# Kernel tuning notes

Hardware: AMD Instinct MI355X
Metric: run time of the kernel (lower is better)

## Reference

```python
import jax, jax.numpy as jnp
import numpy as np


def setup_inputs() -> dict:
    key = jax.random.key(0)
    k1, k2, k3 = jax.random.split(key, 3)
    B, L, C, D, V = 8, 512, 4000, 512, 10000
    x = jax.random.uniform(k1, (B, L, C), dtype=jnp.float32)            # dense char n-gram features
    W_proj = jax.random.normal(k2, (D, C), dtype=jnp.float32) * 0.02     # Linear(char_vsize, d_vec), no bias
    emb_matrix = jax.random.uniform(k3, (V, D), dtype=jnp.float32,
                                    minval=-0.1, maxval=0.1)             # QueryEmb latent embedding table
    return {"x": x, "W_proj": W_proj, "emb_matrix": emb_matrix}


def reference(x, W_proj, emb_matrix):
    # charEmbedder: tanh(Linear(x)) per sentence -> vectorized over batch
    q = jnp.tanh(jnp.einsum('blc,dc->bld', x, W_proj))                   # [B, L, D]
    # QueryEmb: softmax(q @ E^T) @ E + q  (dropout in eval mode = identity)
    attn = jax.nn.softmax(jnp.einsum('bld,vd->blv', q, emb_matrix), axis=-1)  # [B, L, V]
    ctx = jnp.einsum('blv,vd->bld', attn, emb_matrix) + q                # residual
    return ctx
```

## Files before the change

kernel.cpp:

```cpp
#include <hip/hip_runtime.h>
#include <hip/hip_bf16.h>

typedef unsigned short u16;
typedef unsigned int u32;
typedef unsigned char u8;
typedef __bf16 bf16x8 __attribute__((ext_vector_type(8)));
typedef u16 u16x8 __attribute__((ext_vector_type(8)));
typedef float f32x4 __attribute__((ext_vector_type(4)));
typedef u32 u32x4 __attribute__((ext_vector_type(4)));

#define MM   4096
#define CC   4000
#define KP   4096
#define DD   512
#define VV   10000
#define VPAD 10240

#define WS8_QB   0u
#define WS8_QF   4194304u
#define WS8_EF   6291456u
#define WS8_ETF  11534336u
#define WS8_LACC 16777216u
#define WS8_R    16793600u
#define R_XB     0u
#define R_WB     33554432u
#define R_QA     37748736u
#define WS8_PACC 88096768u
#define FAST8_NEED 121651200u

#define WS_Q    0u
#define WS_EB   4194304u
#define WS_ET   14680064u
#define WS_LACC 25165824u
#define WS_P    25182208u

__device__ __forceinline__ u16 f2bf(float f) {
  u32 u = __builtin_bit_cast(u32, f);
  return (u16)((u + 0x7FFFu + ((u >> 16) & 1u)) >> 16);
}
__device__ __forceinline__ float bf2f(u16 h) {
  u32 u = (u32)h << 16;
  return __builtin_bit_cast(float, u);
}
__device__ __forceinline__ u8 f2fp8(float f) {
  u32 u = __builtin_bit_cast(u32, f);
  u32 s = (u >> 31) << 7;
  u32 m = u & 0x7FFFFFFFu;
  if (m < 0x3C800000u) return (u8)s;
  u32 r = m + 0x7FFFFu + ((m >> 20) & 1u);
  return (u8)(((r >> 20) - 960u) | s);
}

#define GLDS(gp, lp) __builtin_amdgcn_global_load_lds( \
    (const __attribute__((address_space(1))) void*)(gp), \
    (__attribute__((address_space(3))) void*)(lp), 16, 0, 0)

__device__ __forceinline__ int fo8(int row, int o) {
  return row * 64 + ((((o >> 1) ^ ((row >> 1) & 3)) << 4) | ((o & 1) << 3));
}


__global__ __launch_bounds__(256) void k_eprep8(const float* __restrict__ E,
                                                u8* __restrict__ Ef,
                                                u8* __restrict__ ETf,
                                                float* __restrict__ Lacc) {
  __shared__ u8 st[64 * 68];
  int tid = threadIdx.x;
  {
    int flat = blockIdx.x * 8 + blockIdx.y;
    int fid = flat * 256 + tid;
    if (fid < MM) Lacc[fid] = 0.f;
  }
  int v0 = blockIdx.x * 64, d0 = blockIdx.y * 64;
  int r = tid >> 2, seg = tid & 3;
  u8 h[16];
  int v = v0 + r;
  if (v < VV) {
    const float* src = E + (size_t)v * DD + d0 + seg * 16;
    #pragma unroll
    for (int j = 0; j < 4; ++j) {
      float4 t = *(const float4*)(src + j * 4);
      h[4*j+0] = f2fp8(t.x * 16.f); h[4*j+1] = f2fp8(t.y * 16.f);
      h[4*j+2] = f2fp8(t.z * 16.f); h[4*j+3] = f2fp8(t.w * 16.f);
    }
  } else {
    #pragma unroll
    for (int j = 0; j < 16; ++j) h[j] = 0;
  }
  {
    u32x4 p;
    #pragma unroll
    for (int q = 0; q < 4; ++q)
      p[q] = (u32)h[4*q] | ((u32)h[4*q+1] << 8) | ((u32)h[4*q+2] << 16) | ((u32)h[4*q+3] << 24);
    *(u32x4*)(Ef + (size_t)v * DD + d0 + seg * 16) = p;
  }
  #pragma unroll
  for (int j = 0; j < 16; ++j) st[r * 68 + seg * 16 + j] = h[j];
  __syncthreads();
  {
    u8 g[16];
    #pragma unroll
    for (int j = 0; j < 16; ++j) g[j] = st[(seg * 16 + j) * 68 + r];
    u32x4 p;
    #pragma unroll
    for (int q = 0; q < 4; ++q)
      p[q] = (u32)g[4*q] | ((u32)g[4*q+1] << 8) | ((u32)g[4*q+2] << 16) | ((u32)g[4*q+3] << 24);
    *(u32x4*)(ETf + (size_t)(d0 + r) * VPAD + v0 + seg * 16) = p;
  }
}

__global__ __launch_bounds__(256) void k_conv(const float* __restrict__ X,
                                              const float* __restrict__ Wp,
                                              u16* __restrict__ Xb,
                                              u16* __restrict__ Wb) {
  int row = blockIdx.x;
  int t = threadIdx.x;
  const float* src;
  u16* dst;
  if (row < MM) { src = X + (size_t)row * CC; dst = Xb + (size_t)row * KP; }
  else { src = Wp + (size_t)(row - MM) * CC; dst = Wb + (size_t)(row - MM) * KP; }
  int c0 = t * 16;
  u16 h[16];
  if (c0 + 16 <= CC) {
    #pragma unroll
    for (int j = 0; j < 4; ++j) {
      float4 v = *(const float4*)(src + c0 + j * 4);
      h[4*j+0] = f2bf(v.x); h[4*j+1] = f2bf(v.y); h[4*j+2] = f2bf(v.z); h[4*j+3] = f2bf(v.w);
    }
  } else {
    #pragma unroll
    for (int j = 0; j < 16; ++j) h[j] = 0;
  }
  u16x8 p0, p1;
  #pragma unroll
  for (int j = 0; j < 8; ++j) { p0[j] = h[j]; p1[j] = h[8+j]; }
  *(u16x8*)(dst + c0) = p0; *(u16x8*)(dst + c0 + 8) = p1;
}

__global__ __launch_bounds__(256) void k_g1(const u16* __restrict__ Xb,
                                            const u16* __restrict__ Wb,
                                            float* __restrict__ Qacc) {
  __shared__ u16 As[128 * 64];
  __shared__ u16 Bs[64 * 64];
  int tid = threadIdx.x;
  int m0 = blockIdx.x * 128;
  int n0 = blockIdx.y * 64;
  int kt0 = blockIdx.z * 16;
  int w = tid >> 6, l = tid & 63;
  int l15 = l & 15, quad = l >> 4;
  int lr = l >> 3, lg = l & 7;
  f32x4 acc[2][4] = {};

  for (int kt = kt0; kt < kt0 + 16; ++kt) {
    #pragma unroll
    for (int i = 0; i < 4; ++i) {
      int wc = i * 4 + w;
      int row = wc * 8 + lr;
      int g = lg ^ (row & 7);
      GLDS(Xb + (size_t)(m0 + row) * KP + kt * 64 + g * 8, As + wc * 512);
      if (i < 2)
        GLDS(Wb + (size_t)(n0 + row) * KP + kt * 64 + g * 8, Bs + wc * 512);
    }
    __syncthreads();
    #pragma unroll
    for (int kk = 0; kk < 2; ++kk) {
      bf16x8 a[2], b[4];
      #pragma unroll
      for (int mi = 0; mi < 2; ++mi) {
        int arow = w * 32 + mi * 16 + l15;
        int slot = (kk * 4 + quad) ^ (arow & 7);
        a[mi] = *(const bf16x8*)&As[arow * 64 + slot * 8];
      }
      #pragma unroll
      for (int ni = 0; ni < 4; ++ni) {
        int brow = ni * 16 + l15;
        int slot = (kk * 4 + quad) ^ (brow & 7);
        b[ni] = *(const bf16x8*)&Bs[brow * 64 + slot * 8];
      }
      #pragma unroll
      for (int mi = 0; mi < 2; ++mi)
        #pragma unroll
        for (int ni = 0; ni < 4; ++ni)
          acc[mi][ni] = __builtin_amdgcn_mfma_f32_16x16x32_bf16(a[mi], b[ni], acc[mi][ni], 0, 0, 0);
    }
    __syncthreads();
  }
  float* dst = Qacc + (size_t)blockIdx.z * (MM * DD);
  #pragma unroll
  for (int mi = 0; mi < 2; ++mi)
    #pragma unroll
    for (int ni = 0; ni < 4; ++ni)
      #pragma unroll
      for (int r = 0; r < 4; ++r) {
        int m = m0 + w * 32 + mi * 16 + quad * 4 + r;
        int d = n0 + ni * 16 + l15;
        dst[(size_t)m * DD + d] = acc[mi][ni][r];
      }
}

__global__ __launch_bounds__(256) void k_tanh4(const float* __restrict__ Qacc,
                                               u16* __restrict__ Qb,
                                               u8* __restrict__ Qf) {
  int idx = blockIdx.x * 256 + threadIdx.x;
  size_t base = (size_t)idx * 8;
  f32x4 s0 = {0,0,0,0}, s1 = {0,0,0,0};
  #pragma unroll
  for (int z = 0; z < 4; ++z) {
    s0 += *(const f32x4*)(Qacc + (size_t)z * (MM * DD) + base);
    s1 += *(const f32x4*)(Qacc + (size_t)z * (MM * DD) + base + 4);
  }
  float t[8];
  #pragma unroll
  for (int j = 0; j < 4; ++j) t[j] = tanhf(s0[j]);
  #pragma unroll
  for (int j = 0; j < 4; ++j) t[4+j] = tanhf(s1[j]);
  u16x8 p;
  #pragma unroll
  for (int j = 0; j < 8; ++j) p[j] = f2bf(t[j]);
  *(u16x8*)(Qb + base) = p;
  unsigned long long q8 = 0;
  #pragma unroll
  for (int j = 0; j < 8; ++j) q8 |= ((unsigned long long)f2fp8(t[j] * 4.f)) << (8 * j);
  *(unsigned long long*)(Qf + base) = q8;
}

__global__ __launch_bounds__(256, 4) void k_s8(const u8* __restrict__ Qf,
                                               const u8* __restrict__ Ef,
                                               u8* __restrict__ Pf,
                                               float* __restrict__ Lacc) {
  __shared__ u8 S8[16384];
  u8* As = S8;
  u8* Bs = S8 + 8192;
  int tid = threadIdx.x;
  int m0 = blockIdx.x * 128;
  int n0 = blockIdx.y * 128;
  int w = tid >> 6, l = tid & 63;
  int l15 = l & 15, quad = l >> 4;
  int mhalf = w >> 1, nhalf = w & 1;
  int srow = tid >> 2, schunk = tid & 3;
  int sw0 = schunk ^ ((srow >> 1) & 3);
  int sw1 = schunk ^ (((srow + 64) >> 1) & 3);
  const u8* qa0 = Qf + (size_t)(m0 + srow) * DD + sw0 * 16;
  const u8* qa1 = Qf + (size_t)(m0 + 64 + srow) * DD + sw1 * 16;
  const u8* eb0 = Ef + (size_t)(n0 + srow) * DD + sw0 * 16;
  const u8* eb1 = Ef + (size_t)(n0 + 64 + srow) * DD + sw1 * 16;
  f32x4 acc[4][4] = {};

  for (int kt = 0; kt < 8; ++kt) {
    GLDS(qa0 + kt * 64, As + tid * 16);
    GLDS(qa1 + kt * 64, As + 4096 + tid * 16);
    GLDS(eb0 + kt * 64, Bs + tid * 16);
    GLDS(eb1 + kt * 64, Bs + 4096 + tid * 16);
    __syncthreads();
    #pragma unroll
    for (int kk = 0; kk < 2; ++kk) {
      long a[4], b[4];
      #pragma unroll
      for (int mi = 0; mi < 4; ++mi) {
        int arow = mhalf * 64 + mi * 16 + l15;
        a[mi] = *(const long*)&As[fo8(arow, kk * 4 + quad)];
      }
      #pragma unroll
      for (int ni = 0; ni < 4; ++ni) {
        int brow = nhalf * 64 + ni * 16 + l15;
        b[ni] = *(const long*)&Bs[fo8(brow, kk * 4 + quad)];
      }
      #pragma unroll
      for (int mi = 0; mi < 4; ++mi)
        #pragma unroll
        for (int ni = 0; ni < 4; ++ni)
          acc[mi][ni] = __builtin_amdgcn_mfma_f32_16x16x32_fp8_fp8(a[mi], b[ni], acc[mi][ni], 0, 0, 0);
    }
    __syncthreads();
  }

  float rs[4][4] = {};
  #pragma unroll
  for (int mi = 0; mi < 4; ++mi) {
    #pragma unroll
    for (int ni = 0; ni < 4; ++ni) {
      int colL = nhalf * 64 + ni * 16 + l15;
      bool ok = (n0 + colL) < VV;
      #pragma unroll
      for (int r = 0; r < 4; ++r) {
        int rowL = mhalf * 64 + mi * 16 + quad * 4 + r;
        float p = ok ? __expf(fminf(acc[mi][ni][r] * 0.015625f, 5.9f)) : 0.f;
        rs[mi][r] += p;
        S8[rowL * 128 + (((colL >> 4) ^ (rowL & 7)) << 4) + (colL & 15)] = f2fp8(p * 0.25f);
      }
    }
  }
  __syncthreads();
  {
    int row = tid >> 1, h2 = tid & 1;
    size_t gbase = (size_t)(m0 + row) * VPAD + n0 + h2 * 64;
    #pragma unroll
    for (int c = 0; c < 4; ++c) {
      int slot = (h2 * 4 + c) ^ (row & 7);
      *(u32x4*)(Pf + gbase + c * 16) = *(const u32x4*)&S8[row * 128 + slot * 16];
    }
  }
  #pragma unroll
  for (int mi = 0; mi < 4; ++mi)
    #pragma unroll
    for (int r = 0; r < 4; ++r) {
      float v = rs[mi][r];
      v += __shfl_xor(v, 1, 16);
      v += __shfl_xor(v, 2, 16);
      v += __shfl_xor(v, 4, 16);
      v += __shfl_xor(v, 8, 16);
      if (l15 == 0)
        atomicAdd(&Lacc[m0 + mhalf * 64 + mi * 16 + quad * 4 + r], v);
    }
}

__global__ __launch_bounds__(256, 4) void k_pvs8(const u8* __restrict__ Pf,
                                                 const u8* __restrict__ ETf,
                                                 float* __restrict__ Pacc) {
  __shared__ u8 S8[16384];
  u8* As = S8;
  u8* Bs = S8 + 8192;
  int tid = threadIdx.x;
  int m0 = blockIdx.x * 128;
  int d0 = blockIdx.y * 128;
  int z = blockIdx.z;
  int w = tid >> 6, l = tid & 63;
  int l15 = l & 15, quad = l >> 4;
  int mhalf = w >> 1, nhalf = w & 1;
  int srow = tid >> 2, schunk = tid & 3;
  int sw0 = schunk ^ ((srow >> 1) & 3);
  int sw1 = schunk ^ (((srow + 64) >> 1) & 3);
  const u8* pa0 = Pf + (size_t)(m0 + srow) * VPAD + sw0 * 16;
  const u8* pa1 = Pf + (size_t)(m0 + 64 + srow) * VPAD + sw1 * 16;
  const u8* eb0 = ETf + (size_t)(d0 + srow) * VPAD + sw0 * 16;
  const u8* eb1 = ETf + (size_t)(d0 + 64 + srow) * VPAD + sw1 * 16;
  f32x4 acc[4][4] = {};
  int kt0 = z * 40;

  for (int kt = kt0; kt < kt0 + 40; ++kt) {
    GLDS(pa0 + kt * 64, As + tid * 16);
    GLDS(pa1 + kt * 64, As + 4096 + tid * 16);
    GLDS(eb0 + kt * 64, Bs + tid * 16);
    GLDS(eb1 + kt * 64, Bs + 4096 + tid * 16);
    __syncthreads();
    #pragma unroll
    for (int kk = 0; kk < 2; ++kk) {
      long a[4], b[4];
      #pragma unroll
      for (int mi = 0; mi < 4; ++mi) {
        int arow = mhalf * 64 + mi * 16 + l15;
        a[mi] = *(const long*)&As[fo8(arow, kk * 4 + quad)];
      }
      #pragma unroll
      for (int ni = 0; ni < 4; ++ni) {
        int brow = nhalf * 64 + ni * 16 + l15;
        b[ni] = *(const long*)&Bs[fo8(brow, kk * 4 + quad)];
      }
      #pragma unroll
      for (int mi = 0; mi < 4; ++mi)
        #pragma unroll
        for (int ni = 0; ni < 4; ++ni)
          acc[mi][ni] = __builtin_amdgcn_mfma_f32_16x16x32_fp8_fp8(a[mi], b[ni], acc[mi][ni], 0, 0, 0);
    }
    __syncthreads();
  }
  float* dst = Pacc + (size_t)z * (MM * DD);
  #pragma unroll
  for (int mi = 0; mi < 4; ++mi)
    #pragma unroll
    for (int ni = 0; ni < 4; ++ni)
      #pragma unroll
      for (int r = 0; r < 4; ++r) {
        int m = m0 + mhalf * 64 + mi * 16 + quad * 4 + r;
        int d = d0 + nhalf * 64 + ni * 16 + l15;
        dst[(size_t)m * DD + d] = acc[mi][ni][r];
      }
}

__global__ __launch_bounds__(256) void k_fin4(float* __restrict__ Out,
                                              const float* __restrict__ Lacc,
                                              const u16* __restrict__ Qb,
                                              const float* __restrict__ Pacc) {
  int idx = blockIdx.x * 256 + threadIdx.x;
  int m = idx >> 7;
  int d4 = (idx & 127) * 4;
  float inv = 0.25f / Lacc[m];
  size_t off = (size_t)m * DD + d4;
  f32x4 s = {0.f, 0.f, 0.f, 0.f};
  #pragma unroll
  for (int z = 0; z < 4; ++z)
    s += *(const f32x4*)(Pacc + (size_t)z * (MM * DD) + off);
  const u16* qp = Qb + off;
  f32x4 r;
  #pragma unroll
  for (int i = 0; i < 4; ++i) r[i] = s[i] * inv + bf2f(qp[i]);
  *(f32x4*)(Out + off) = r;
}


__global__ __launch_bounds__(256) void k_eprep(const float* __restrict__ E,
                                               u16* __restrict__ Eb,
                                               u16* __restrict__ ETb,
                                               float* __restrict__ Out,
                                               float* __restrict__ Lacc) {
  __shared__ u16 st[64 * 65];
  int tid = threadIdx.x;
  {
    int bid = blockIdx.x * 8 + blockIdx.y;
    f32x4 z = {0.f, 0.f, 0.f, 0.f};
    #pragma unroll
    for (int rep = 0; rep < 2; ++rep) {
      int id = bid * 256 + tid + rep * 327680;
      if (id < 524288)      *(f32x4*)(Out + (size_t)id * 4) = z;
      else if (id < 525312) *(f32x4*)(Lacc + (size_t)(id - 524288) * 4) = z;
    }
  }
  int v0 = blockIdx.x * 64, d0 = blockIdx.y * 64;
  int r = tid >> 2, seg = tid & 3;
  u16 h[16];
  int v = v0 + r;
  if (v < VV) {
    const float* src = E + (size_t)v * DD + d0 + seg * 16;
    #pragma unroll
    for (int j = 0; j < 4; ++j) {
      float4 t = *(const float4*)(src + j * 4);
      h[4*j+0] = f2bf(t.x); h[4*j+1] = f2bf(t.y); h[4*j+2] = f2bf(t.z); h[4*j+3] = f2bf(t.w);
    }
  } else {
    #pragma unroll
    for (int j = 0; j < 16; ++j) h[j] = 0;
  }
  {
    u16x8 p0, p1;
    #pragma unroll
    for (int j = 0; j < 8; ++j) { p0[j] = h[j]; p1[j] = h[8+j]; }
    u16* dst = Eb + (size_t)v * DD + d0 + seg * 16;
    *(u16x8*)dst = p0; *(u16x8*)(dst + 8) = p1;
  }
  #pragma unroll
  for (int j = 0; j < 16; ++j) st[r * 65 + seg * 16 + j] = h[j];
  __syncthreads();
  {
    u16 g[16];
    #pragma unroll
    for (int j = 0; j < 16; ++j) g[j] = st[(seg * 16 + j) * 65 + r];
    u16x8 p0, p1;
    #pragma unroll
    for (int j = 0; j < 8; ++j) { p0[j] = g[j]; p1[j] = g[8+j]; }
    u16* dst = ETb + (size_t)(d0 + r) * VPAD + v0 + seg * 16;
    *(u16x8*)dst = p0; *(u16x8*)(dst + 8) = p1;
  }
}

__global__ __launch_bounds__(256) void k_gemm1(const float* __restrict__ X,
                                               const float* __restrict__ W,
                                               u16* __restrict__ Qb) {
  __shared__ u16 xs[64 * 64];
  __shared__ u16 wst[64 * 64];
  int tid = threadIdx.x;
  int m0 = blockIdx.x * 64;
  int n0 = blockIdx.y * 64;
  int srow = tid >> 2;
  int sseg = tid & 3;
  int r7 = srow & 7;
  const float* xsrc = X + (size_t)(m0 + srow) * CC + sseg * 16;
  const float* wsrc = W + (size_t)(n0 + srow) * CC + sseg * 16;
  int lane = tid & 63;
  int wv = tid >> 6;
  int l15 = lane & 15, quad = lane >> 4;
  f32x4 acc[4] = {};

  for (int kt = 0; kt < 63; ++kt) {
    int cbase = kt * 64 + sseg * 16;
    float xv[16], wf[16];
    if (cbase + 16 <= CC) {
      #pragma unroll
      for (int j = 0; j < 4; ++j) {
        float4 tx = *(const float4*)(xsrc + kt * 64 + j * 4);
        float4 tw = *(const float4*)(wsrc + kt * 64 + j * 4);
        xv[4*j+0] = tx.x; xv[4*j+1] = tx.y; xv[4*j+2] = tx.z; xv[4*j+3] = tx.w;
        wf[4*j+0] = tw.x; wf[4*j+1] = tw.y; wf[4*j+2] = tw.z; wf[4*j+3] = tw.w;
      }
    } else {
      #pragma unroll
      for (int j = 0; j < 16; ++j) { xv[j] = 0.f; wf[j] = 0.f; }
    }
    __syncthreads();
    #pragma unroll
    for (int j = 0; j < 2; ++j) {
      int g = (sseg * 2 + j) ^ r7;
      u16x8 px, pw;
      #pragma unroll
      for (int e = 0; e < 8; ++e) { px[e] = f2bf(xv[8*j+e]); pw[e] = f2bf(wf[8*j+e]); }
      *(u16x8*)&xs[srow * 64 + (g << 3)] = px;
      *(u16x8*)&wst[srow * 64 + (g << 3)] = pw;
    }
    __syncthreads();
    #pragma unroll
    for (int kk = 0; kk < 2; ++kk) {
      int arow = 16 * wv + l15;
      int ga = (kk * 4 + quad) ^ (arow & 7);
      bf16x8 a = *(const bf16x8*)&xs[arow * 64 + (ga << 3)];
      #pragma unroll
      for (int nb = 0; nb < 4; ++nb) {
        int brow = 16 * nb + l15;
        int gb = (kk * 4 + quad) ^ (brow & 7);
        bf16x8 b = *(const bf16x8*)&wst[brow * 64 + (gb << 3)];
        acc[nb] = __builtin_amdgcn_mfma_f32_16x16x32_bf16(a, b, acc[nb], 0, 0, 0);
      }
    }
  }
  #pragma unroll
  for (int nb = 0; nb < 4; ++nb) {
    int d = n0 + 16 * nb + l15;
    #pragma unroll
    for (int r = 0; r < 4; ++r) {
      int m = m0 + 16 * wv + 4 * quad + r;
      Qb[(size_t)m * DD + d] = f2bf(tanhf(acc[nb][r]));
    }
  }
}

__global__ __launch_bounds__(256) void k_s(const u16* __restrict__ Qb,
                                           const u16* __restrict__ Eb,
                                           u16* __restrict__ Pg,
                                           float* __restrict__ Lacc,
                                           int cbase, int W) {
  __shared__ u16 As[128 * 64];
  __shared__ u16 Bs[128 * 64];
  int tid = threadIdx.x;
  int m0 = blockIdx.x * 128;
  int n0 = blockIdx.y * 128;
  int w = tid >> 6, l = tid & 63;
  int l15 = l & 15, quad = l >> 4;
  int mhalf = w >> 1, nhalf = w & 1;
  int lr = l >> 3, lg = l & 7;
  f32x4 acc[4][4] = {};

  for (int kt = 0; kt < 8; ++kt) {
    #pragma unroll
    for (int i = 0; i < 4; ++i) {
      int wc = i * 4 + w;
      int row = wc * 8 + lr;
      int g = lg ^ (row & 7);
      GLDS(Qb + (size_t)(m0 + row) * DD + kt * 64 + g * 8, As + wc * 512);
      GLDS(Eb + (size_t)(cbase + n0 + row) * DD + kt * 64 + g * 8, Bs + wc * 512);
    }
    __syncthreads();
    #pragma unroll
    for (int kk = 0; kk < 2; ++kk) {
      bf16x8 a[4], b[4];
      #pragma unroll
      for (int mi = 0; mi < 4; ++mi) {
        int arow = mhalf * 64 + mi * 16 + l15;
        int slot = (kk * 4 + quad) ^ (arow & 7);
        a[mi] = *(const bf16x8*)&As[arow * 64 + slot * 8];
      }
      #pragma unroll
      for (int ni = 0; ni < 4; ++ni) {
        int brow = nhalf * 64 + ni * 16 + l15;
        int slot = (kk * 4 + quad) ^ (brow & 7);
        b[ni] = *(const bf16x8*)&Bs[brow * 64 + slot * 8];
      }
      #pragma unroll
      for (int mi = 0; mi < 4; ++mi)
        #pragma unroll
        for (int ni = 0; ni < 4; ++ni)
          acc[mi][ni] = __builtin_amdgcn_mfma_f32_16x16x32_bf16(a[mi], b[ni], acc[mi][ni], 0, 0, 0);
    }
    __syncthreads();
  }

  float rs[4][4] = {};
  #pragma unroll
  for (int mi = 0; mi < 4; ++mi) {
    #pragma unroll
    for (int ni = 0; ni < 4; ++ni) {
      int ncol = n0 + nhalf * 64 + ni * 16 + l15;
      bool ok = (cbase + ncol) < VV;
      #pragma unroll
      for (int r = 0; r < 4; ++r) {
        float p = ok ? __expf(acc[mi][ni][r]) : 0.f;
        rs[mi][r] += p;
        int m = m0 + mhalf * 64 + mi * 16 + quad * 4 + r;
        Pg[(size_t)m * W + ncol] = f2bf(p);
      }
    }
  }
  #pragma unroll
  for (int mi = 0; mi < 4; ++mi)
    #pragma unroll
    for (int r = 0; r < 4; ++r) {
      float v = rs[mi][r];
      v += __shfl_xor(v, 1, 16);
      v += __shfl_xor(v, 2, 16);
      v += __shfl_xor(v, 4, 16);
      v += __shfl_xor(v, 8, 16);
      if (l15 == 0)
        atomicAdd(&Lacc[m0 + mhalf * 64 + mi * 16 + quad * 4 + r], v);
    }
}

__global__ __launch_bounds__(256) void k_pv(const u16* __restrict__ Pg,
                                            const u16* __restrict__ ETb,
                                            float* __restrict__ Out,
                                            int cbase, int W) {
  __shared__ u16 As[128 * 64];
  __shared__ u16 Bs[64 * 64];
  int tid = threadIdx.x;
  int m0 = blockIdx.x * 128;
  int n0 = blockIdx.y * 64;
  int w = tid >> 6, l = tid & 63;
  int l15 = l & 15, quad = l >> 4;
  int lr = l >> 3, lg = l & 7;
  int iters = W >> 6;
  f32x4 acc[2][4] = {};

  for (int kt = 0; kt < iters; ++kt) {
    #pragma unroll
    for (int i = 0; i < 4; ++i) {
      int wc = i * 4 + w;
      int row = wc * 8 + lr;
      int g = lg ^ (row & 7);
      GLDS(Pg + (size_t)(m0 + row) * W + kt * 64 + g * 8, As + wc * 512);
      if (i < 2)
        GLDS(ETb + (size_t)(n0 + row) * VPAD + cbase + kt * 64 + g * 8, Bs + wc * 512);
    }
    __syncthreads();
    #pragma unroll
    for (int kk = 0; kk < 2; ++kk) {
      bf16x8 a[2], b[4];
      #pragma unroll
      for (int mi = 0; mi < 2; ++mi) {
        int arow = w * 32 + mi * 16 + l15;
        int slot = (kk * 4 + quad) ^ (arow & 7);
        a[mi] = *(const bf16x8*)&As[arow * 64 + slot * 8];
      }
      #pragma unroll
      for (int ni = 0; ni < 4; ++ni) {
        int brow = ni * 16 + l15;
        int slot = (kk * 4 + quad) ^ (brow & 7);
        b[ni] = *(const bf16x8*)&Bs[brow * 64 + slot * 8];
      }
      #pragma unroll
      for (int mi = 0; mi < 2; ++mi)
        #pragma unroll
        for (int ni = 0; ni < 4; ++ni)
          acc[mi][ni] = __builtin_amdgcn_mfma_f32_16x16x32_bf16(a[mi], b[ni], acc[mi][ni], 0, 0, 0);
    }
    __syncthreads();
  }
  #pragma unroll
  for (int mi = 0; mi < 2; ++mi)
    #pragma unroll
    for (int ni = 0; ni < 4; ++ni)
      #pragma unroll
      for (int r = 0; r < 4; ++r) {
        int m = m0 + w * 32 + mi * 16 + quad * 4 + r;
        int d = n0 + ni * 16 + l15;
        Out[(size_t)m * DD + d] += acc[mi][ni][r];
      }
}

__global__ __launch_bounds__(256) void k_fin(float* __restrict__ Out,
                                             const float* __restrict__ Lacc,
                                             const u16* __restrict__ Qb) {
  int idx = blockIdx.x * 256 + threadIdx.x;
  int m = idx >> 7;
  int d4 = (idx & 127) * 4;
  float inv = 1.f / Lacc[m];
  f32x4 ov = *(const f32x4*)(Out + (size_t)m * DD + d4);
  const u16* qp = Qb + (size_t)m * DD + d4;
  f32x4 r;
  #pragma unroll
  for (int i = 0; i < 4; ++i) r[i] = ov[i] * inv + bf2f(qp[i]);
  *(f32x4*)(Out + (size_t)m * DD + d4) = r;
}

extern "C" void kernel_launch(void* const* d_in, const int* in_sizes, int n_in,
                              void* d_out, int out_size, void* d_ws, size_t ws_size,
                              hipStream_t stream) {
  const float* x  = (const float*)d_in[0];
  const float* Wp = (const float*)d_in[1];
  const float* E  = (const float*)d_in[2];
  float* out = (float*)d_out;
  char* ws = (char*)d_ws;

  if (ws_size >= (size_t)FAST8_NEED) {
    u16*   Qb   = (u16*)(ws + WS8_QB);
    u8*    Qf   = (u8*)(ws + WS8_QF);
    u8*    Ef   = (u8*)(ws + WS8_EF);
    u8*    ETf  = (u8*)(ws + WS8_ETF);
    float* Lacc = (float*)(ws + WS8_LACC);
    u16*   Xb   = (u16*)(ws + WS8_R + R_XB);
    u16*   Wb   = (u16*)(ws + WS8_R + R_WB);
    float* Qacc = (float*)(ws + WS8_R + R_QA);
    u8*    Pf   = (u8*)(ws + WS8_R);
    float* Pacc = (float*)(ws + WS8_PACC);

    k_eprep8<<<dim3(VPAD / 64, DD / 64), 256, 0, stream>>>(E, Ef, ETf, Lacc);
    k_conv<<<dim3(MM + DD), 256, 0, stream>>>(x, Wp, Xb, Wb);
    k_g1<<<dim3(MM / 128, DD / 64, 4), 256, 0, stream>>>(Xb, Wb, Qacc);
    k_tanh4<<<dim3(MM * DD / 8 / 256), 256, 0, stream>>>(Qacc, Qb, Qf);
    k_s8<<<dim3(MM / 128, VPAD / 128), 256, 0, stream>>>(Qf, Ef, Pf, Lacc);
    k_pvs8<<<dim3(MM / 128, DD / 128, 4), 256, 0, stream>>>(Pf, ETf, Pacc);
    k_fin4<<<dim3(MM * DD / 4 / 256), 256, 0, stream>>>(out, Lacc, Qb, Pacc);
  } else {
    u16*   Qb   = (u16*)(ws + WS_Q);
    u16*   Eb   = (u16*)(ws + WS_EB);
    u16*   ETb  = (u16*)(ws + WS_ET);
    float* Lacc = (float*)(ws + WS_LACC);
    u16*   Pc   = (u16*)(ws + WS_P);
    int W = 640;
    if (ws_size >= (size_t)WS_P + (size_t)MM * 2560 * 2) W = 2560;
    else if (ws_size >= (size_t)WS_P + (size_t)MM * 1280 * 2) W = 1280;
    int nch = VPAD / W;
    k_eprep<<<dim3(VPAD / 64, DD / 64), 256, 0, stream>>>(E, Eb, ETb, out, Lacc);
    k_gemm1<<<dim3(MM / 64, DD / 64), 256, 0, stream>>>(x, Wp, Qb);
    for (int c = 0; c < nch; ++c) {
      k_s <<<dim3(MM / 128, W / 128), 256, 0, stream>>>(Qb, Eb, Pc, Lacc, c * W, W);
      k_pv<<<dim3(MM / 128, DD / 64), 256, 0, stream>>>(Pc, ETb, out, c * W, W);
    }
    k_fin<<<dim3(MM * DD / 4 / 256), 256, 0, stream>>>(out, Lacc, Qb);
  }
}
```

Before: 272.8 us.

## Permute fp8 K layout for 16-byte LDS reads, packed cvt, split PV 8-way

Stores the fp8 Q, E and E^T buffers with a permuted byte order inside each 64-byte group, so each lane fetches both MFMA k-halves with a single 16-byte LDS read instead of two 8-byte reads. It also uses the hardware packed fp8 convert where available, rewrites the softmax exponent as exp2 with a fused scale and offset (which changes the P scaling), and splits the PV reduction into 8 K-chunks instead of 4 for more parallelism. The price is a larger workspace requirement (the fast path may be skipped if the workspace is too small), more partial-sum traffic in the final kernel, and the risk that the permuted layout does not match the P tiles written by k_s8.

Result: faster. 256.9 us (-5.8%).

```diff
diff --git a/kernel.cpp b/kernel.cpp
--- a/kernel.cpp
+++ b/kernel.cpp
@@ -8,6 +8,8 @@
 typedef u16 u16x8 __attribute__((ext_vector_type(8)));
 typedef float f32x4 __attribute__((ext_vector_type(4)));
 typedef u32 u32x4 __attribute__((ext_vector_type(4)));
+typedef u32 u32x2 __attribute__((ext_vector_type(2)));
+typedef long longx2 __attribute__((ext_vector_type(2)));
 
 #define MM   4096
 #define CC   4000
@@ -26,7 +28,7 @@
 #define R_WB     33554432u
 #define R_QA     37748736u
 #define WS8_PACC 88096768u
-#define FAST8_NEED 121651200u
+#define FAST8_NEED 155205632u
 
 #define WS_Q    0u
 #define WS_EB   4194304u
@@ -50,14 +52,26 @@
   u32 r = m + 0x7FFFFu + ((m >> 20) & 1u);
   return (u8)(((r >> 20) - 960u) | s);
 }
+__device__ __forceinline__ u32 pk4fp8(float f0, float f1, float f2, float f3) {
+#if __has_builtin(__builtin_amdgcn_cvt_pk_fp8_f32)
+  int w = 0;
+  w = __builtin_amdgcn_cvt_pk_fp8_f32(f0, f1, w, false);
+  w = __builtin_amdgcn_cvt_pk_fp8_f32(f2, f3, w, true);
+  return (u32)w;
+#else
+  return (u32)f2fp8(f0) | ((u32)f2fp8(f1) << 8) |
+         ((u32)f2fp8(f2) << 16) | ((u32)f2fp8(f3) << 24);
+#endif
+}
 
 #define GLDS(gp, lp) __builtin_amdgcn_global_load_lds( \
     (const __attribute__((address_space(1))) void*)(gp), \
     (__attribute__((address_space(3))) void*)(lp), 16, 0, 0)
 
-__device__ __forceinline__ int fo8(int row, int o) {
-  return row * 64 + ((((o >> 1) ^ ((row >> 1) & 3)) << 4) | ((o & 1) << 3));
-}
+__device__ __forceinline__ int fr16(int row, int q) {
+  return row * 64 + (((q ^ ((row >> 1) & 3)) << 4));
+}
+__device__ __forceinline__ int pgrp(int j) { return (j & 3) * 2 + (j >> 2); }
 
 
 __global__ __launch_bounds__(256) void k_eprep8(const float* __restrict__ E,
@@ -73,39 +87,42 @@
   }
   int v0 = blockIdx.x * 64, d0 = blockIdx.y * 64;
   int r = tid >> 2, seg = tid & 3;
-  u8 h[16];
+  u32 w[4];
   int v = v0 + r;
   if (v < VV) {
     const float* src = E + (size_t)v * DD + d0 + seg * 16;
     #pragma unroll
     for (int j = 0; j < 4; ++j) {
       float4 t = *(const float4*)(src + j * 4);
-      h[4*j+0] = f2fp8(t.x * 16.f); h[4*j+1] = f2fp8(t.y * 16.f);
-      h[4*j+2] = f2fp8(t.z * 16.f); h[4*j+3] = f2fp8(t.w * 16.f);
+      w[j] = pk4fp8(t.x * 16.f, t.y * 16.f, t.z * 16.f, t.w * 16.f);
     }
   } else {
     #pragma unroll
-    for (int j = 0; j < 16; ++j) h[j] = 0;
-  }
+    for (int j = 0; j < 4; ++j) w[j] = 0;
+  }
+  int g0 = pgrp(2 * seg), g1 = pgrp(2 * seg + 1);
   {
-    u32x4 p;
-    #pragma unroll
-    for (int q = 0; q < 4; ++q)
-      p[q] = (u32)h[4*q] | ((u32)h[4*q+1] << 8) | ((u32)h[4*q+2] << 16) | ((u32)h[4*q+3] << 24);
-    *(u32x4*)(Ef + (size_t)v * DD + d0 + seg * 16) = p;
-  }
-  #pragma unroll
-  for (int j = 0; j < 16; ++j) st[r * 68 + seg * 16 + j] = h[j];
+    size_t rowb = (size_t)v * DD + d0;
+    u32x2 a = {w[0], w[1]}, b = {w[2], w[3]};
+    *(u32x2*)(Ef + rowb + g0 * 8) = a;
+    *(u32x2*)(Ef + rowb + g1 * 8) = b;
+  }
+  #pragma unroll
+  for (int j = 0; j < 4; ++j)
+    *(u32*)&st[r * 68 + seg * 16 + j * 4] = w[j];
   __syncthreads();
   {
     u8 g[16];
     #pragma unroll
     for (int j = 0; j < 16; ++j) g[j] = st[(seg * 16 + j) * 68 + r];
-    u32x4 p;
+    u32 t[4];
     #pragma unroll
     for (int q = 0; q < 4; ++q)
-      p[q] = (u32)g[4*q] | ((u32)g[4*q+1] << 8) | ((u32)g[4*q+2] << 16) | ((u32)g[4*q+3] << 24);
-    *(u32x4*)(ETf + (size_t)(d0 + r) * VPAD + v0 + seg * 16) = p;
+      t[q] = (u32)g[4*q] | ((u32)g[4*q+1] << 8) | ((u32)g[4*q+2] << 16) | ((u32)g[4*q+3] << 24);
+    size_t rowb = (size_t)(d0 + r) * VPAD + v0;
+    u32x2 a = {t[0], t[1]}, b = {t[2], t[3]};
+    *(u32x2*)(ETf + rowb + g0 * 8) = a;
+    *(u32x2*)(ETf + rowb + g1 * 8) = b;
   }
 }
 
@@ -218,10 +235,12 @@
   #pragma unroll
   for (int j = 0; j < 8; ++j) p[j] = f2bf(t[j]);
   *(u16x8*)(Qb + base) = p;
-  unsigned long long q8 = 0;
-  #pragma unroll
-  for (int j = 0; j < 8; ++j) q8 |= ((unsigned long long)f2fp8(t[j] * 4.f)) << (8 * j);
-  *(unsigned long long*)(Qf + base) = q8;
+  u32x2 q8;
+  q8[0] = pk4fp8(t[0] * 4.f, t[1] * 4.f, t[2] * 4.f, t[3] * 4.f);
+  q8[1] = pk4fp8(t[4] * 4.f, t[5] * 4.f, t[6] * 4.f, t[7] * 4.f);
+  int jg = (int)((base >> 3) & 7);
+  size_t dest = (base & ~(size_t)63) + (size_t)pgrp(jg) * 8;
+  *(u32x2*)(Qf + dest) = q8;
 }
 
 __global__ __launch_bounds__(256, 4) void k_s8(const u8* __restrict__ Qf,
@@ -238,12 +257,11 @@
   int l15 = l & 15, quad = l >> 4;
   int mhalf = w >> 1, nhalf = w & 1;
   int srow = tid >> 2, schunk = tid & 3;
-  int sw0 = schunk ^ ((srow >> 1) & 3);
-  int sw1 = schunk ^ (((srow + 64) >> 1) & 3);
-  const u8* qa0 = Qf + (size_t)(m0 + srow) * DD + sw0 * 16;
-  const u8* qa1 = Qf + (size_t)(m0 + 64 + srow) * DD + sw1 * 16;
-  const u8* eb0 = Ef + (size_t)(n0 + srow) * DD + sw0 * 16;
-  const u8* eb1 = Ef + (size_t)(n0 + 64 + srow) * DD + sw1 * 16;
+  int sw = schunk ^ ((srow >> 1) & 3);
+  const u8* qa0 = Qf + (size_t)(m0 + srow) * DD + sw * 16;
+  const u8* qa1 = Qf + (size_t)(m0 + 64 + srow) * DD + sw * 16;
+  const u8* eb0 = Ef + (size_t)(n0 + srow) * DD + sw * 16;
+  const u8* eb1 = Ef + (size_t)(n0 + 64 + srow) * DD + sw * 16;
   f32x4 acc[4][4] = {};
 
   for (int kt = 0; kt < 8; ++kt) {
@@ -252,41 +270,49 @@
     GLDS(eb0 + kt * 64, Bs + tid * 16);
     GLDS(eb1 + kt * 64, Bs + 4096 + tid * 16);
     __syncthreads();
-    #pragma unroll
-    for (int kk = 0; kk < 2; ++kk) {
-      long a[4], b[4];
-      #pragma unroll
-      for (int mi = 0; mi < 4; ++mi) {
-        int arow = mhalf * 64 + mi * 16 + l15;
-        a[mi] = *(const long*)&As[fo8(arow, kk * 4 + quad)];
-      }
-      #pragma unroll
-      for (int ni = 0; ni < 4; ++ni) {
-        int brow = nhalf * 64 + ni * 16 + l15;
-        b[ni] = *(const long*)&Bs[fo8(brow, kk * 4 + quad)];
-      }
-      #pragma unroll
-      for (int mi = 0; mi < 4; ++mi)
-        #pragma unroll
-        for (int ni = 0; ni < 4; ++ni)
-          acc[mi][ni] = __builtin_amdgcn_mfma_f32_16x16x32_fp8_fp8(a[mi], b[ni], acc[mi][ni], 0, 0, 0);
-    }
-    __syncthreads();
-  }
-
+    longx2 a[4], b[4];
+    #pragma unroll
+    for (int mi = 0; mi < 4; ++mi)
+      a[mi] = *(const longx2*)&As[fr16(mhalf * 64 + mi * 16 + l15, quad)];
+    #pragma unroll
+    for (int ni = 0; ni < 4; ++ni)
+      b[ni] = *(const longx2*)&Bs[fr16(nhalf * 64 + ni * 16 + l15, quad)];
+    #pragma unroll
+    for (int mi = 0; mi < 4; ++mi)
+      #pragma unroll
+      for (int ni = 0; ni < 4; ++ni)
+        acc[mi][ni] = __builtin_amdgcn_mfma_f32_16x16x32_fp8_fp8(a[mi][0], b[ni][0], acc[mi][ni], 0, 0, 0);
+    #pragma unroll
+    for (int mi = 0; mi < 4; ++mi)
+      #pragma unroll
+      for (int ni = 0; ni < 4; ++ni)
+        acc[mi][ni] = __builtin_amdgcn_mfma_f32_16x16x32_fp8_fp8(a[mi][1], b[ni][1], acc[mi][ni], 0, 0, 0);
+    __syncthreads();
+  }
+
+  const float C2 = 0.0225421100138901f;
   float rs[4][4] = {};
   #pragma unroll
   for (int mi = 0; mi < 4; ++mi) {
     #pragma unroll
     for (int ni = 0; ni < 4; ++ni) {
-      int colL = nhalf * 64 + ni * 16 + l15;
-      bool ok = (n0 + colL) < VV;
+      bool ok = (n0 + nhalf * 64 + ni * 16 + l15) < VV;
+      int p_in = ((ni & 1) * 2 + (l15 >> 3)) * 16 + ((ni >> 1) << 3) + (l15 & 7);
+      int gbyte = nhalf * 64 + p_in;
+      int gch = gbyte >> 4, glo = gbyte & 15;
+      float pf[4];
+      #pragma unroll
+      for (int r = 0; r < 4; ++r) {
+        float t = fminf(fmaf(acc[mi][ni][r], C2, -2.f), 6.3f);
+        float p = ok ? exp2f(t) : 0.f;
+        pf[r] = p;
+        rs[mi][r] += p;
+      }
+      u32 wpk = pk4fp8(pf[0], pf[1], pf[2], pf[3]);
       #pragma unroll
       for (int r = 0; r < 4; ++r) {
         int rowL = mhalf * 64 + mi * 16 + quad * 4 + r;
-        float p = ok ? __expf(fminf(acc[mi][ni][r] * 0.015625f, 5.9f)) : 0.f;
-        rs[mi][r] += p;
-        S8[rowL * 128 + (((colL >> 4) ^ (rowL & 7)) << 4) + (colL & 15)] = f2fp8(p * 0.25f);
+        S8[rowL * 128 + ((gch ^ (rowL & 7)) << 4) + glo] = (u8)(wpk >> (8 * r));
       }
     }
   }
@@ -296,8 +322,9 @@
     size_t gbase = (size_t)(m0 + row) * VPAD + n0 + h2 * 64;
     #pragma unroll
     for (int c = 0; c < 4; ++c) {
-      int slot = (h2 * 4 + c) ^ (row & 7);
-      *(u32x4*)(Pf + gbase + c * 16) = *(const u32x4*)&S8[row * 128 + slot * 16];
+      int slot = h2 * 4 + c;
+      *(u32x4*)(Pf + gbase + c * 16) =
+          *(const u32x4*)&S8[row * 128 + ((slot ^ (row & 7)) << 4)];
     }
   }
   #pragma unroll
@@ -328,40 +355,37 @@
   int l15 = l & 15, quad = l >> 4;
   int mhalf = w >> 1, nhalf = w & 1;
   int srow = tid >> 2, schunk = tid & 3;
-  int sw0 = schunk ^ ((srow >> 1) & 3);
-  int sw1 = schunk ^ (((srow + 64) >> 1) & 3);
-  const u8* pa0 = Pf + (size_t)(m0 + srow) * VPAD + sw0 * 16;
-  const u8* pa1 = Pf + (size_t)(m0 + 64 + srow) * VPAD + sw1 * 16;
-  const u8* eb0 = ETf + (size_t)(d0 + srow) * VPAD + sw0 * 16;
-  const u8* eb1 = ETf + (size_t)(d0 + 64 + srow) * VPAD + sw1 * 16;
+  int sw = schunk ^ ((srow >> 1) & 3);
+  const u8* pa0 = Pf + (size_t)(m0 + srow) * VPAD + sw * 16;
+  const u8* pa1 = Pf + (size_t)(m0 + 64 + srow) * VPAD + sw * 16;
+  const u8* eb0 = ETf + (size_t)(d0 + srow) * VPAD + sw * 16;
+  const u8* eb1 = ETf + (size_t)(d0 + 64 + srow) * VPAD + sw * 16;
   f32x4 acc[4][4] = {};
-  int kt0 = z * 40;
-
-  for (int kt = kt0; kt < kt0 + 40; ++kt) {
+  int kt0 = z * 20;
+
+  for (int kt = kt0; kt < kt0 + 20; ++kt) {
     GLDS(pa0 + kt * 64, As + tid * 16);
     GLDS(pa1 + kt * 64, As + 4096 + tid * 16);
     GLDS(eb0 + kt * 64, Bs + tid * 16);
     GLDS(eb1 + kt * 64, Bs + 4096 + tid * 16);
     __syncthreads();
-    #pragma unroll
-    for (int kk = 0; kk < 2; ++kk) {
-      long a[4], b[4];
-      #pragma unroll
-      for (int mi = 0; mi < 4; ++mi) {
-        int arow = mhalf * 64 + mi * 16 + l15;
-        a[mi] = *(const long*)&As[fo8(arow, kk * 4 + quad)];
-      }
-      #pragma unroll
-      for (int ni = 0; ni < 4; ++ni) {
-        int brow = nhalf * 64 + ni * 16 + l15;
-        b[ni] = *(const long*)&Bs[fo8(brow, kk * 4 + quad)];
-      }
-      #pragma unroll
-      for (int mi = 0; mi < 4; ++mi)
-        #pragma unroll
-        for (int ni = 0; ni < 4; ++ni)
-          acc[mi][ni] = __builtin_amdgcn_mfma_f32_16x16x32_fp8_fp8(a[mi], b[ni], acc[mi][ni], 0, 0, 0);
-    }
+    longx2 a[4], b[4];
+    #pragma unroll
+    for (int mi = 0; mi < 4; ++mi)
+      a[mi] = *(const longx2*)&As[fr16(mhalf * 64 + mi * 16 + l15, quad)];
+    #pragma unroll
+    for (int ni = 0; ni < 4; ++ni)
+      b[ni] = *(const longx2*)&Bs[fr16(nhalf * 64 + ni * 16 + l15, quad)];
+    #pragma unroll
+    for (int mi = 0; mi < 4; ++mi)
+      #pragma unroll
+      for (int ni = 0; ni < 4; ++ni)
+        acc[mi][ni] = __builtin_amdgcn_mfma_f32_16x16x32_fp8_fp8(a[mi][0], b[ni][0], acc[mi][ni], 0, 0, 0);
+    #pragma unroll
+    for (int mi = 0; mi < 4; ++mi)
+      #pragma unroll
+      for (int ni = 0; ni < 4; ++ni)
+        acc[mi][ni] = __builtin_amdgcn_mfma_f32_16x16x32_fp8_fp8(a[mi][1], b[ni][1], acc[mi][ni], 0, 0, 0);
     __syncthreads();
   }
   float* dst = Pacc + (size_t)z * (MM * DD);
@@ -377,18 +401,18 @@
       }
 }
 
-__global__ __launch_bounds__(256) void k_fin4(float* __restrict__ Out,
-                                              const float* __restrict__ Lacc,
-                                              const u16* __restrict__ Qb,
-                                              const float* __restrict__ Pacc) {
+__global__ __launch_bounds__(256) void k_fin8v2(float* __restrict__ Out,
+                                                const float* __restrict__ Lacc,
+                                                const u16* __restrict__ Qb,
+                                                const float* __restrict__ Pacc) {
   int idx = blockIdx.x * 256 + threadIdx.x;
   int m = idx >> 7;
   int d4 = (idx & 127) * 4;
-  float inv = 0.25f / Lacc[m];
+  float inv = 0.0625f / Lacc[m];
   size_t off = (size_t)m * DD + d4;
   f32x4 s = {0.f, 0.f, 0.f, 0.f};
   #pragma unroll
-  for (int z = 0; z < 4; ++z)
+  for (int z = 0; z < 8; ++z)
     s += *(const f32x4*)(Pacc + (size_t)z * (MM * DD) + off);
   const u16* qp = Qb + off;
   f32x4 r;
@@ -703,8 +727,8 @@
     k_g1<<<dim3(MM / 128, DD / 64, 4), 256, 0, stream>>>(Xb, Wb, Qacc);
     k_tanh4<<<dim3(MM * DD / 8 / 256), 256, 0, stream>>>(Qacc, Qb, Qf);
     k_s8<<<dim3(MM / 128, VPAD / 128), 256, 0, stream>>>(Qf, Ef, Pf, Lacc);
-    k_pvs8<<<dim3(MM / 128, DD / 128, 4), 256, 0, stream>>>(Pf, ETf, Pacc);
-    k_fin4<<<dim3(MM * DD / 4 / 256), 256, 0, stream>>>(out, Lacc, Qb, Pacc);
+    k_pvs8<<<dim3(MM / 128, DD / 128, 8), 256, 0, stream>>>(Pf, ETf, Pacc);
+    k_fin8v2<<<dim3(MM * DD / 4 / 256), 256, 0, stream>>>(out, Lacc, Qb, Pacc);
   } else {
     u16*   Qb   = (u16*)(ws + WS_Q);
     u16*   Eb   = (u16*)(ws + WS_EB);
```
